# Optimization experiments

Hardware: AMD Instinct MI355X
Metric: run time of the kernel (lower is better)

Reference implementation:

```python
import jax, jax.numpy as jnp
import numpy as np

NEG_BIG = -1e9

def setup_inputs() -> dict:
    key = jax.random.key(0)
    kq, kk, kv, kwq, kwk, kwv, km = jax.random.split(key, 7)
    B, S, d = 16, 1024, 512
    Q = jax.random.normal(kq, (B, S, d), dtype=jnp.float32)
    K = jax.random.normal(kk, (B, S, d), dtype=jnp.float32)
    V = jax.random.normal(kv, (B, S, d), dtype=jnp.float32)
    # nn.Linear weights [d, d]; torch applies x @ W.T
    WQ = jax.random.normal(kwq, (d, d), dtype=jnp.float32) / np.sqrt(d)
    WK = jax.random.normal(kwk, (d, d), dtype=jnp.float32) / np.sqrt(d)
    WV = jax.random.normal(kwv, (d, d), dtype=jnp.float32) / np.sqrt(d)
    mask = jax.random.randint(km, (B, S), 0, 2, dtype=jnp.int32)
    return {"Q": Q, "K": K, "V": V, "WQ": WQ, "WK": WK, "WV": WV, "mask": mask}


def reference(Q, K, V, WQ, WK, WV, mask):
    d = Q.shape[-1]
    q = jnp.einsum('bsd,ed->bse', Q, WQ)
    k = jnp.einsum('bsd,ed->bse', K, WK)
    v = jnp.einsum('bsd,ed->bse', V, WV)
    scores = jnp.einsum('bqd,bkd->bqk', q, k) / jnp.sqrt(jnp.float32(d))
    attn = jax.nn.softmax(scores, axis=-1)
    # Faithful to original: mask applied AFTER softmax with -1e9 fill
    m = mask[:, None, :]  # [B,1,S] broadcast over query dim
    attn = jnp.where(m == 0, jnp.float32(NEG_BIG), attn)
    out = jnp.einsum('bqk,bkd->bqd', attn, v)
    return (out, attn)
```

## Files before the change

### kernel.cpp

```cpp
#include <hip/hip_runtime.h>
#include <hip/hip_bf16.h>

typedef float f32x4 __attribute__((ext_vector_type(4)));
typedef __bf16 bf16x8 __attribute__((ext_vector_type(8)));
typedef unsigned short u16x8 __attribute__((ext_vector_type(8)));
typedef unsigned short u16x4 __attribute__((ext_vector_type(4)));
typedef int i32x4 __attribute__((ext_vector_type(4)));

#define NEG_BIG_F (-1000000000.0f)
#define SCALE_F 0.044194173824159216f

__device__ __forceinline__ unsigned short f2bf(float f) {
  unsigned int u = __float_as_uint(f);
  u += 0x7FFFu + ((u >> 16) & 1u);
  return (unsigned short)(u >> 16);
}

__device__ __forceinline__ u16x8 cvt8(f32x4 a, f32x4 b) {
  u16x8 r;
  r[0] = f2bf(a[0]); r[1] = f2bf(a[1]); r[2] = f2bf(a[2]); r[3] = f2bf(a[3]);
  r[4] = f2bf(b[0]); r[5] = f2bf(b[1]); r[6] = f2bf(b[2]); r[7] = f2bf(b[3]);
  return r;
}

__device__ __forceinline__ bf16x8 u2b(u16x8 u) {
  union { u16x8 u; bf16x8 b; } c; c.u = u; return c.b;
}

__device__ __forceinline__ void gload16(const void* g, char* l) {
  __builtin_amdgcn_global_load_lds(
      (const __attribute__((address_space(1))) unsigned int*)g,
      (__attribute__((address_space(3))) unsigned int*)l, 16, 0, 0);
}

__global__ __launch_bounds__(256) void cvtW(
    const float* __restrict__ w0, const float* __restrict__ w1,
    const float* __restrict__ w2, unsigned short* __restrict__ out)
{
  const float* src = blockIdx.z == 0 ? w0 : (blockIdx.z == 1 ? w1 : w2);
  unsigned short* dst = out + (size_t)blockIdx.z * 262144;
  const int i = (blockIdx.x * 256 + threadIdx.x) * 8;
  f32x4 a = *(const f32x4*)(src + i);
  f32x4 b = *(const f32x4*)(src + i + 4);
  *(u16x8*)&dst[i] = cvt8(a, b);
}

__global__ __launch_bounds__(512, 2) void projqk(
    const float* __restrict__ Q, const float* __restrict__ Kx,
    const unsigned short* __restrict__ wb,
    unsigned short* __restrict__ qb, unsigned short* __restrict__ kb)
{
  __shared__ __align__(16) unsigned short As[2][256][32];
  __shared__ __align__(16) unsigned short Bs[2][256][32];

  const int tid = threadIdx.x, z = blockIdx.z;
  const float* X = z ? Kx : Q;
  const unsigned short* W = wb + (size_t)z * 262144;
  unsigned short* Y = z ? kb : qb;
  const int m0 = blockIdx.x * 256, n0 = blockIdx.y * 256;
  const int lane = tid & 63, wave = tid >> 6;
  const int wr = (wave >> 2) * 128, wc = (wave & 3) * 64;
  const int fr = lane & 15, fq = lane >> 4;

  f32x4 acc[8][4] = {};

  int arow_s[2], aswz_s[2];
  const float* gAs[2];
  #pragma unroll
  for (int i = 0; i < 2; i++) {
    const int c = tid + 512 * i;
    arow_s[i] = c >> 2;
    aswz_s[i] = ((c & 3) ^ ((arow_s[i] >> 1) & 3)) * 8;
    gAs[i] = X + (size_t)(m0 + arow_s[i]) * 512 + (c & 3) * 8;
  }
  const unsigned short* gB[2]; char* lB[2];
  #pragma unroll
  for (int i = 0; i < 2; i++) {
    const int c = tid + 512 * i, row = c >> 2, slot = c & 3;
    gB[i] = W + (size_t)(n0 + row) * 512 + (slot ^ ((row >> 1) & 3)) * 8;
    lB[i] = (char*)&Bs[0][0][0] + c * 16;
  }

  f32x4 pa[2][2];
  #pragma unroll
  for (int i = 0; i < 2; i++) {
    pa[i][0] = *(const f32x4*)(gAs[i]);
    pa[i][1] = *(const f32x4*)(gAs[i] + 4);
  }
  #pragma unroll
  for (int i = 0; i < 2; i++) gload16(gB[i], lB[i]);
  #pragma unroll
  for (int i = 0; i < 2; i++)
    *(u16x8*)&As[0][arow_s[i]][aswz_s[i]] = cvt8(pa[i][0], pa[i][1]);

  int cur = 0;
  for (int kt = 0; kt < 512; kt += 32) {
    const int nb = cur ^ 1;
    if (kt < 480) {
      #pragma unroll
      for (int i = 0; i < 2; i++) {
        pa[i][0] = *(const f32x4*)(gAs[i] + kt + 32);
        pa[i][1] = *(const f32x4*)(gAs[i] + kt + 36);
      }
      #pragma unroll
      for (int i = 0; i < 2; i++) gload16(gB[i] + kt + 32, lB[i] + nb * 16384);
      asm volatile("s_waitcnt vmcnt(6) lgkmcnt(0)" ::: "memory");
    } else {
      asm volatile("s_waitcnt vmcnt(0) lgkmcnt(0)" ::: "memory");
    }
    __builtin_amdgcn_sched_barrier(0);
    __builtin_amdgcn_s_barrier();

    bf16x8 bv[4];
    #pragma unroll
    for (int nf = 0; nf < 4; nf++) {
      const int br = wc + nf * 16 + fr;
      bv[nf] = *(const bf16x8*)&Bs[cur][br][(fq ^ ((br >> 1) & 3)) * 8];
    }
    #pragma unroll
    for (int mf = 0; mf < 8; mf++) {
      const int ar = wr + mf * 16 + fr;
      bf16x8 av = *(const bf16x8*)&As[cur][ar][(fq ^ ((ar >> 1) & 3)) * 8];
      #pragma unroll
      for (int nf = 0; nf < 4; nf++)
        acc[mf][nf] = __builtin_amdgcn_mfma_f32_16x16x32_bf16(av, bv[nf], acc[mf][nf], 0, 0, 0);
    }

    if (kt < 480) {
      #pragma unroll
      for (int i = 0; i < 2; i++)
        *(u16x8*)&As[nb][arow_s[i]][aswz_s[i]] = cvt8(pa[i][0], pa[i][1]);
    }
    __builtin_amdgcn_s_barrier();
    cur = nb;
  }

  #pragma unroll
  for (int mf = 0; mf < 8; mf++)
    #pragma unroll
    for (int nf = 0; nf < 4; nf++)
      #pragma unroll
      for (int rr = 0; rr < 4; rr++) {
        const int m = m0 + wr + mf * 16 + fq * 4 + rr;
        const int n = n0 + wc + nf * 16 + fr;
        Y[(size_t)m * 512 + n] = f2bf(acc[mf][nf][rr]);
      }
}

__global__ __launch_bounds__(512, 2) void projv(
    const float* __restrict__ V, const unsigned short* __restrict__ wv,
    unsigned short* __restrict__ vt)
{
  __shared__ __align__(16) unsigned short As[2][128][32];
  __shared__ __align__(16) unsigned short Bs[2][256][32];

  const int tid = threadIdx.x;
  const int m0 = blockIdx.x * 128, n0 = blockIdx.y * 256, b = blockIdx.z;
  const int lane = tid & 63, wave = tid >> 6;
  const int wr = (wave >> 2) * 64, wc = (wave & 3) * 64;
  const int fr = lane & 15, fq = lane >> 4;

  f32x4 acc[4][4] = {};

  const int ar_s = tid >> 2, aslot = tid & 3;
  const unsigned short* gA = wv + (size_t)(m0 + ar_s) * 512 + (aslot ^ ((ar_s >> 1) & 3)) * 8;
  char* lA = (char*)&As[0][0][0] + tid * 16;

  int brow_s[2], bswz_s[2];
  const float* gBs[2];
  #pragma unroll
  for (int i = 0; i < 2; i++) {
    const int c = tid + 512 * i;
    brow_s[i] = c >> 2;
    bswz_s[i] = ((c & 3) ^ ((brow_s[i] >> 1) & 3)) * 8;
    gBs[i] = V + ((size_t)b * 1024 + n0 + brow_s[i]) * 512 + (c & 3) * 8;
  }

  f32x4 pb[2][2];
  #pragma unroll
  for (int i = 0; i < 2; i++) {
    pb[i][0] = *(const f32x4*)(gBs[i]);
    pb[i][1] = *(const f32x4*)(gBs[i] + 4);
  }
  gload16(gA, lA);
  #pragma unroll
  for (int i = 0; i < 2; i++)
    *(u16x8*)&Bs[0][brow_s[i]][bswz_s[i]] = cvt8(pb[i][0], pb[i][1]);

  int cur = 0;
  for (int kt = 0; kt < 512; kt += 32) {
    const int nb = cur ^ 1;
    if (kt < 480) {
      #pragma unroll
      for (int i = 0; i < 2; i++) {
        pb[i][0] = *(const f32x4*)(gBs[i] + kt + 32);
        pb[i][1] = *(const f32x4*)(gBs[i] + kt + 36);
      }
      gload16(gA + kt + 32, lA + nb * 8192);
      asm volatile("s_waitcnt vmcnt(5) lgkmcnt(0)" ::: "memory");
    } else {
      asm volatile("s_waitcnt vmcnt(0) lgkmcnt(0)" ::: "memory");
    }
    __builtin_amdgcn_sched_barrier(0);
    __builtin_amdgcn_s_barrier();

    bf16x8 av[4], bv[4];
    #pragma unroll
    for (int mf = 0; mf < 4; mf++) {
      const int ar = wr + mf * 16 + fr;
      av[mf] = *(const bf16x8*)&As[cur][ar][(fq ^ ((ar >> 1) & 3)) * 8];
    }
    #pragma unroll
    for (int nf = 0; nf < 4; nf++) {
      const int br = wc + nf * 16 + fr;
      bv[nf] = *(const bf16x8*)&Bs[cur][br][(fq ^ ((br >> 1) & 3)) * 8];
    }
    #pragma unroll
    for (int mf = 0; mf < 4; mf++)
      #pragma unroll
      for (int nf = 0; nf < 4; nf++)
        acc[mf][nf] = __builtin_amdgcn_mfma_f32_16x16x32_bf16(av[mf], bv[nf], acc[mf][nf], 0, 0, 0);

    if (kt < 480) {
      #pragma unroll
      for (int i = 0; i < 2; i++)
        *(u16x8*)&Bs[nb][brow_s[i]][bswz_s[i]] = cvt8(pb[i][0], pb[i][1]);
    }
    __builtin_amdgcn_s_barrier();
    cur = nb;
  }

  #pragma unroll
  for (int mf = 0; mf < 4; mf++)
    #pragma unroll
    for (int nf = 0; nf < 4; nf++)
      #pragma unroll
      for (int rr = 0; rr < 4; rr++) {
        const int e = m0 + wr + mf * 16 + fq * 4 + rr;
        const int s = n0 + wc + nf * 16 + fr;
        vt[((size_t)b * 512 + e) * 1024 + s] = f2bf(acc[mf][nf][rr]);
      }
}

__global__ __launch_bounds__(512, 2) void score256(
    const unsigned short* __restrict__ qb, const unsigned short* __restrict__ kb,
    float* __restrict__ attn, float* __restrict__ partial)
{
  __shared__ __align__(16) unsigned short As[2][256][32];
  __shared__ __align__(16) unsigned short Bs[2][256][32];

  const int tid = threadIdx.x, bz = blockIdx.z;
  const int m0 = blockIdx.x * 256, n0 = blockIdx.y * 256;
  const int lane = tid & 63, wave = tid >> 6;
  const int wr = (wave >> 2) * 128, wc = (wave & 3) * 64;
  const int fr = lane & 15, fq = lane >> 4;

  f32x4 acc[8][4] = {};

  const unsigned short* gA[2]; char* lA[2];
  const unsigned short* gB[2]; char* lB[2];
  #pragma unroll
  for (int i = 0; i < 2; i++) {
    const int c = tid + 512 * i, row = c >> 2, slot = c & 3;
    const int sw = (slot ^ ((row >> 1) & 3)) * 8;
    gA[i] = qb + ((size_t)bz * 1024 + m0 + row) * 512 + sw;
    gB[i] = kb + ((size_t)bz * 1024 + n0 + row) * 512 + sw;
    lA[i] = (char*)&As[0][0][0] + c * 16;
    lB[i] = (char*)&Bs[0][0][0] + c * 16;
  }

  #pragma unroll
  for (int i = 0; i < 2; i++) { gload16(gA[i], lA[i]); gload16(gB[i], lB[i]); }

  int cur = 0;
  for (int kt = 0; kt < 512; kt += 32) {
    const int nb = cur ^ 1;
    if (kt < 480) {
      #pragma unroll
      for (int i = 0; i < 2; i++) {
        gload16(gA[i] + kt + 32, lA[i] + nb * 16384);
        gload16(gB[i] + kt + 32, lB[i] + nb * 16384);
      }
      asm volatile("s_waitcnt vmcnt(4) lgkmcnt(0)" ::: "memory");
    } else {
      asm volatile("s_waitcnt vmcnt(0) lgkmcnt(0)" ::: "memory");
    }
    __builtin_amdgcn_sched_barrier(0);
    __builtin_amdgcn_s_barrier();

    bf16x8 bv[4];
    #pragma unroll
    for (int nf = 0; nf < 4; nf++) {
      const int br = wc + nf * 16 + fr;
      bv[nf] = *(const bf16x8*)&Bs[cur][br][(fq ^ ((br >> 1) & 3)) * 8];
    }
    #pragma unroll
    for (int mf = 0; mf < 8; mf++) {
      const int ar = wr + mf * 16 + fr;
      bf16x8 av = *(const bf16x8*)&As[cur][ar][(fq ^ ((ar >> 1) & 3)) * 8];
      #pragma unroll
      for (int nf = 0; nf < 4; nf++)
        acc[mf][nf] = __builtin_amdgcn_mfma_f32_16x16x32_bf16(av, bv[nf], acc[mf][nf], 0, 0, 0);
    }
    __builtin_amdgcn_s_barrier();
    cur = nb;
  }

  float* Cb = attn + (size_t)bz * 1024 * 1024;
  const int slot = blockIdx.y * 4 + (wave & 3);
  #pragma unroll
  for (int mf = 0; mf < 8; mf++) {
    #pragma unroll
    for (int rr = 0; rr < 4; rr++) {
      const int m = m0 + wr + mf * 16 + fq * 4 + rr;
      float e = 0.f;
      #pragma unroll
      for (int nf = 0; nf < 4; nf++) {
        const float sv = acc[mf][nf][rr] * SCALE_F;
        Cb[(size_t)m * 1024 + n0 + wc + nf * 16 + fr] = sv;
        e += __expf(sv);
      }
      e += __shfl_xor(e, 1); e += __shfl_xor(e, 2);
      e += __shfl_xor(e, 4); e += __shfl_xor(e, 8);
      if (fr == 0)
        partial[(size_t)slot * 16384 + bz * 1024 + m] = e;
    }
  }
}

__global__ __launch_bounds__(256) void rs_inv(
    const float* __restrict__ partial, float* __restrict__ inv)
{
  const int i = blockIdx.x * 256 + threadIdx.x;
  float s = 0.f;
  #pragma unroll
  for (int p = 0; p < 16; p++) s += partial[(size_t)p * 16384 + i];
  inv[i] = 1.0f / s;
}

__global__ __launch_bounds__(512) void pv_gemm(
    float* __restrict__ attn, const unsigned short* __restrict__ vt,
    const float* __restrict__ inv, const int* __restrict__ mask,
    float* __restrict__ out)
{
  __shared__ __align__(16) unsigned short As[2][64][40];
  __shared__ __align__(16) unsigned short Bs[2][512][32];

  const int tid = threadIdx.x;
  const int bz = blockIdx.z, m0 = blockIdx.x * 64;
  const int lane = tid & 63, wave = tid >> 6;
  const int n0 = wave * 64;
  const int fr = lane & 15, fq = lane >> 4;

  f32x4 acc[4][4] = {};

  const int arow = tid >> 3, acol = (tid & 7) * 4;
  float* arp = attn + ((size_t)bz * 1024 + m0 + arow) * 1024 + acol;
  const float vinv = inv[bz * 1024 + m0 + arow];
  const int* mrow = mask + bz * 1024 + acol;

  const unsigned short* gB[4];
  char* lB[4];
  #pragma unroll
  for (int r = 0; r < 4; r++) {
    const int c = r * 512 + tid;
    const int row = c >> 2;
    gB[r] = vt + ((size_t)bz * 512 + row) * 1024 + ((c & 3) ^ ((row >> 1) & 3)) * 8;
    lB[r] = (char*)&Bs[0][0][0] + c * 16;
  }

  {
    f32x4 s = *(const f32x4*)(arp);
    i32x4 mv = *(const i32x4*)(mrow);
    f32x4 p;
    p[0] = mv[0] ? __expf(s[0]) * vinv : NEG_BIG_F;
    p[1] = mv[1] ? __expf(s[1]) * vinv : NEG_BIG_F;
    p[2] = mv[2] ? __expf(s[2]) * vinv : NEG_BIG_F;
    p[3] = mv[3] ? __expf(s[3]) * vinv : NEG_BIG_F;
    *(f32x4*)(arp) = p;
    u16x4 h;
    h[0] = f2bf(p[0]); h[1] = f2bf(p[1]); h[2] = f2bf(p[2]); h[3] = f2bf(p[3]);
    *(u16x4*)&As[0][arow][acol] = h;
    #pragma unroll
    for (int r = 0; r < 4; r++) gload16(gB[r], lB[r]);
  }
  __syncthreads();

  int cur = 0;
  for (int kt = 0; kt < 1024; kt += 32) {
    const int nb = cur ^ 1;
    f32x4 s; i32x4 mv;
    const bool more = (kt + 32) < 1024;
    if (more) {
      s = *(const f32x4*)(arp + kt + 32);
      mv = *(const i32x4*)(mrow + kt + 32);
      #pragma unroll
      for (int r = 0; r < 4; r++) gload16(gB[r] + kt + 32, lB[r] + nb * 32768);
    }

    bf16x8 af[4], bv[4];
    #pragma unroll
    for (int t = 0; t < 4; t++) {
      af[t] = *(const bf16x8*)&As[cur][t * 16 + fr][fq * 8];
      const int brow = n0 + t * 16 + fr;
      bv[t] = *(const bf16x8*)&Bs[cur][brow][(fq ^ ((brow >> 1) & 3)) * 8];
    }
    #pragma unroll
    for (int mt = 0; mt < 4; mt++)
      #pragma unroll
      for (int nt = 0; nt < 4; nt++)
        acc[mt][nt] = __builtin_amdgcn_mfma_f32_16x16x32_bf16(af[mt], bv[nt], acc[mt][nt], 0, 0, 0);

    if (more) {
      f32x4 p;
      p[0] = mv[0] ? __expf(s[0]) * vinv : NEG_BIG_F;
      p[1] = mv[1] ? __expf(s[1]) * vinv : NEG_BIG_F;
      p[2] = mv[2] ? __expf(s[2]) * vinv : NEG_BIG_F;
      p[3] = mv[3] ? __expf(s[3]) * vinv : NEG_BIG_F;
      *(f32x4*)(arp + kt + 32) = p;
      u16x4 h;
      h[0] = f2bf(p[0]); h[1] = f2bf(p[1]); h[2] = f2bf(p[2]); h[3] = f2bf(p[3]);
      *(u16x4*)&As[nb][arow][acol] = h;
    }
    __syncthreads();
    cur = nb;
  }

  #pragma unroll
  for (int mt = 0; mt < 4; mt++)
    #pragma unroll
    for (int nt = 0; nt < 4; nt++)
      #pragma unroll
      for (int rr = 0; rr < 4; rr++)
        out[((size_t)bz * 1024 + m0 + mt * 16 + fq * 4 + rr) * 512 + n0 + nt * 16 + fr] =
            acc[mt][nt][rr];
}

extern "C" void kernel_launch(void* const* d_in, const int* in_sizes, int n_in,
                              void* d_out, int out_size, void* d_ws, size_t ws_size,
                              hipStream_t stream)
{
  const float* Q  = (const float*)d_in[0];
  const float* Kx = (const float*)d_in[1];
  const float* V  = (const float*)d_in[2];
  const float* WQ = (const float*)d_in[3];
  const float* WK = (const float*)d_in[4];
  const float* WV = (const float*)d_in[5];
  const int* mask = (const int*)d_in[6];

  const int B = 16, S = 1024, D = 512;
  float* out_f  = (float*)d_out;
  float* attn_f = out_f + (size_t)B * S * D;

  unsigned short* qb = (unsigned short*)d_ws;
  unsigned short* kb = qb + (size_t)B * S * D;
  unsigned short* vt = kb + (size_t)B * S * D;
  unsigned short* wb = vt + (size_t)B * S * D;
  float* partial = (float*)(wb + 786432);
  float* inv = partial + 262144;

  cvtW<<<dim3(128, 1, 3), 256, 0, stream>>>(WQ, WK, WV, wb);
  projqk<<<dim3(64, 2, 2), 512, 0, stream>>>(Q, Kx, wb, qb, kb);
  projv<<<dim3(4, 4, 16), 512, 0, stream>>>(V, wb + 524288, vt);
  score256<<<dim3(4, 4, 16), 512, 0, stream>>>(qb, kb, attn_f, partial);
  rs_inv<<<dim3(64), 256, 0, stream>>>(partial, inv);
  pv_gemm<<<dim3(16, 1, 16), 512, 0, stream>>>(attn_f, vt, inv, mask, out_f);
}
```

Measured before the change: 163.5 us.

## Store masked unnormalized bf16 probabilities and fold the mask term algebraically into the PV output

score256 now applies exp and the mask and writes unnormalized bf16 probabilities into the output buffer, instead of writing fp32 scores. A separate attn_write kernel builds the normalized fp32 attn output from them. pv_gemm streams that bf16 P with async global_load_lds double buffering and adds the contribution of the -1e9 masked entries algebraically, using a per-column masked V sum from a new mvsum_k kernel. The aim is to cut the fp32 read-modify-write of the full attention matrix and the per-element exp inside the GEMM loop. In exchange it adds two kernel launches, reuses the output memory as scratch (safe only because each block reads exactly the rows it later overwrites), and changes rounding of the large masked term.

```diff
diff --git a/kernel.cpp b/kernel.cpp
--- a/kernel.cpp
+++ b/kernel.cpp
@@ -4,7 +4,6 @@
 typedef float f32x4 __attribute__((ext_vector_type(4)));
 typedef __bf16 bf16x8 __attribute__((ext_vector_type(8)));
 typedef unsigned short u16x8 __attribute__((ext_vector_type(8)));
-typedef unsigned short u16x4 __attribute__((ext_vector_type(4)));
 typedef int i32x4 __attribute__((ext_vector_type(4)));
 
 #define NEG_BIG_F (-1000000000.0f)
@@ -14,6 +13,10 @@
   unsigned int u = __float_as_uint(f);
   u += 0x7FFFu + ((u >> 16) & 1u);
   return (unsigned short)(u >> 16);
+}
+
+__device__ __forceinline__ float bf2f(unsigned short h) {
+  return __uint_as_float((unsigned int)h << 16);
 }
 
 __device__ __forceinline__ u16x8 cvt8(f32x4 a, f32x4 b) {
@@ -21,10 +24,6 @@
   r[0] = f2bf(a[0]); r[1] = f2bf(a[1]); r[2] = f2bf(a[2]); r[3] = f2bf(a[3]);
   r[4] = f2bf(b[0]); r[5] = f2bf(b[1]); r[6] = f2bf(b[2]); r[7] = f2bf(b[3]);
   return r;
-}
-
-__device__ __forceinline__ bf16x8 u2b(u16x8 u) {
-  union { u16x8 u; bf16x8 b; } c; c.u = u; return c.b;
 }
 
 __device__ __forceinline__ void gload16(const void* g, char* l) {
@@ -244,7 +243,8 @@
 
 __global__ __launch_bounds__(512, 2) void score256(
     const unsigned short* __restrict__ qb, const unsigned short* __restrict__ kb,
-    float* __restrict__ attn, float* __restrict__ partial)
+    const int* __restrict__ mask,
+    unsigned short* __restrict__ P, float* __restrict__ partial)
 {
   __shared__ __align__(16) unsigned short As[2][256][32];
   __shared__ __align__(16) unsigned short Bs[2][256][32];
@@ -306,7 +306,12 @@
     cur = nb;
   }
 
-  float* Cb = attn + (size_t)bz * 1024 * 1024;
+  int mcol[4];
+  #pragma unroll
+  for (int nf = 0; nf < 4; nf++)
+    mcol[nf] = mask[bz * 1024 + n0 + wc + nf * 16 + fr];
+
+  unsigned short* Pb = P + ((size_t)bz << 20);
   const int slot = blockIdx.y * 4 + (wave & 3);
   #pragma unroll
   for (int mf = 0; mf < 8; mf++) {
@@ -316,9 +321,10 @@
       float e = 0.f;
       #pragma unroll
       for (int nf = 0; nf < 4; nf++) {
-        const float sv = acc[mf][nf][rr] * SCALE_F;
-        Cb[(size_t)m * 1024 + n0 + wc + nf * 16 + fr] = sv;
-        e += __expf(sv);
+        const float ev = __expf(acc[mf][nf][rr] * SCALE_F);
+        e += ev;
+        Pb[(size_t)m * 1024 + n0 + wc + nf * 16 + fr] =
+            mcol[nf] ? f2bf(ev) : (unsigned short)0;
       }
       e += __shfl_xor(e, 1); e += __shfl_xor(e, 2);
       e += __shfl_xor(e, 4); e += __shfl_xor(e, 8);
@@ -338,12 +344,60 @@
   inv[i] = 1.0f / s;
 }
 
+__global__ __launch_bounds__(256) void mvsum_k(
+    const unsigned short* __restrict__ vt, const int* __restrict__ mask,
+    float* __restrict__ mvsum)
+{
+  const int row = blockIdx.x * 4 + (threadIdx.x >> 6);
+  const int b = row >> 9;
+  const int lane = threadIdx.x & 63;
+  const unsigned short* vr = vt + (size_t)row * 1024 + lane * 16;
+  const int* mr = mask + b * 1024 + lane * 16;
+  u16x8 v0 = *(const u16x8*)(vr);
+  u16x8 v1 = *(const u16x8*)(vr + 8);
+  float s = 0.f;
+  #pragma unroll
+  for (int j = 0; j < 8; j++) {
+    if (!mr[j])     s += bf2f(v0[j]);
+    if (!mr[8 + j]) s += bf2f(v1[j]);
+  }
+  #pragma unroll
+  for (int o = 32; o > 0; o >>= 1) s += __shfl_xor(s, o);
+  if (lane == 0) mvsum[row] = s;
+}
+
+__global__ __launch_bounds__(256) void attn_write(
+    const unsigned short* __restrict__ P, const float* __restrict__ inv,
+    const int* __restrict__ mask, float* __restrict__ attn)
+{
+  const size_t base = ((size_t)blockIdx.x * 256 + threadIdx.x) * 8;
+  const int row = (int)(base >> 10);
+  const int b = row >> 10;
+  const int k0 = (int)(base & 1023);
+  const u16x8 p8 = *(const u16x8*)(P + base);
+  const float iv = inv[row];
+  const int* mr = mask + b * 1024 + k0;
+  const i32x4 ma = *(const i32x4*)(mr);
+  const i32x4 mb = *(const i32x4*)(mr + 4);
+  f32x4 o0, o1;
+  o0[0] = ma[0] ? bf2f(p8[0]) * iv : NEG_BIG_F;
+  o0[1] = ma[1] ? bf2f(p8[1]) * iv : NEG_BIG_F;
+  o0[2] = ma[2] ? bf2f(p8[2]) * iv : NEG_BIG_F;
+  o0[3] = ma[3] ? bf2f(p8[3]) * iv : NEG_BIG_F;
+  o1[0] = mb[0] ? bf2f(p8[4]) * iv : NEG_BIG_F;
+  o1[1] = mb[1] ? bf2f(p8[5]) * iv : NEG_BIG_F;
+  o1[2] = mb[2] ? bf2f(p8[6]) * iv : NEG_BIG_F;
+  o1[3] = mb[3] ? bf2f(p8[7]) * iv : NEG_BIG_F;
+  *(f32x4*)(attn + base) = o0;
+  *(f32x4*)(attn + base + 4) = o1;
+}
+
 __global__ __launch_bounds__(512) void pv_gemm(
-    float* __restrict__ attn, const unsigned short* __restrict__ vt,
-    const float* __restrict__ inv, const int* __restrict__ mask,
+    const unsigned short* __restrict__ P, const unsigned short* __restrict__ vt,
+    const float* __restrict__ inv, const float* __restrict__ mvsum,
     float* __restrict__ out)
 {
-  __shared__ __align__(16) unsigned short As[2][64][40];
+  __shared__ __align__(16) unsigned short As[2][64][32];
   __shared__ __align__(16) unsigned short Bs[2][512][32];
 
   const int tid = threadIdx.x;
@@ -354,86 +408,75 @@
 
   f32x4 acc[4][4] = {};
 
-  const int arow = tid >> 3, acol = (tid & 7) * 4;
-  float* arp = attn + ((size_t)bz * 1024 + m0 + arow) * 1024 + acol;
-  const float vinv = inv[bz * 1024 + m0 + arow];
-  const int* mrow = mask + bz * 1024 + acol;
-
-  const unsigned short* gB[4];
-  char* lB[4];
-  #pragma unroll
-  for (int r = 0; r < 4; r++) {
-    const int c = r * 512 + tid;
-    const int row = c >> 2;
-    gB[r] = vt + ((size_t)bz * 512 + row) * 1024 + ((c & 3) ^ ((row >> 1) & 3)) * 8;
-    lB[r] = (char*)&Bs[0][0][0] + c * 16;
-  }
-
-  {
-    f32x4 s = *(const f32x4*)(arp);
-    i32x4 mv = *(const i32x4*)(mrow);
-    f32x4 p;
-    p[0] = mv[0] ? __expf(s[0]) * vinv : NEG_BIG_F;
-    p[1] = mv[1] ? __expf(s[1]) * vinv : NEG_BIG_F;
-    p[2] = mv[2] ? __expf(s[2]) * vinv : NEG_BIG_F;
-    p[3] = mv[3] ? __expf(s[3]) * vinv : NEG_BIG_F;
-    *(f32x4*)(arp) = p;
-    u16x4 h;
-    h[0] = f2bf(p[0]); h[1] = f2bf(p[1]); h[2] = f2bf(p[2]); h[3] = f2bf(p[3]);
-    *(u16x4*)&As[0][arow][acol] = h;
-    #pragma unroll
-    for (int r = 0; r < 4; r++) gload16(gB[r], lB[r]);
-  }
-  __syncthreads();
+  const unsigned short* gA = nullptr; char* lA = nullptr;
+  if (tid < 256) {
+    const int row = tid >> 2, slot = tid & 3;
+    gA = P + ((size_t)bz << 20) + (size_t)(m0 + row) * 1024 + (slot ^ ((row >> 1) & 3)) * 8;
+    lA = (char*)&As[0][0][0] + tid * 16;
+  }
+  const unsigned short* gB[4]; char* lB[4];
+  #pragma unroll
+  for (int i = 0; i < 4; i++) {
+    const int c = tid + 512 * i, row = c >> 2, slot = c & 3;
+    gB[i] = vt + ((size_t)bz * 512 + row) * 1024 + (slot ^ ((row >> 1) & 3)) * 8;
+    lB[i] = (char*)&Bs[0][0][0] + c * 16;
+  }
+
+  if (tid < 256) gload16(gA, lA);
+  #pragma unroll
+  for (int i = 0; i < 4; i++) gload16(gB[i], lB[i]);
 
   int cur = 0;
-  for (int kt = 0; kt < 1024; kt += 32) {
+  for (int t = 0; t < 32; t++) {
     const int nb = cur ^ 1;
-    f32x4 s; i32x4 mv;
-    const bool more = (kt + 32) < 1024;
-    if (more) {
-      s = *(const f32x4*)(arp + kt + 32);
-      mv = *(const i32x4*)(mrow + kt + 32);
-      #pragma unroll
-      for (int r = 0; r < 4; r++) gload16(gB[r] + kt + 32, lB[r] + nb * 32768);
-    }
+    const int kt = t * 32;
+    if (t < 31) {
+      if (tid < 256) gload16(gA + kt + 32, lA + nb * 4096);
+      #pragma unroll
+      for (int i = 0; i < 4; i++) gload16(gB[i] + kt + 32, lB[i] + nb * 32768);
+      if (wave < 4) asm volatile("s_waitcnt vmcnt(5) lgkmcnt(0)" ::: "memory");
+      else          asm volatile("s_waitcnt vmcnt(4) lgkmcnt(0)" ::: "memory");
+    } else {
+      asm volatile("s_waitcnt vmcnt(0) lgkmcnt(0)" ::: "memory");
+    }
+    __builtin_amdgcn_sched_barrier(0);
+    __builtin_amdgcn_s_barrier();
 
     bf16x8 af[4], bv[4];
     #pragma unroll
-    for (int t = 0; t < 4; t++) {
-      af[t] = *(const bf16x8*)&As[cur][t * 16 + fr][fq * 8];
-      const int brow = n0 + t * 16 + fr;
-      bv[t] = *(const bf16x8*)&Bs[cur][brow][(fq ^ ((brow >> 1) & 3)) * 8];
-    }
-    #pragma unroll
-    for (int mt = 0; mt < 4; mt++)
-      #pragma unroll
-      for (int nt = 0; nt < 4; nt++)
-        acc[mt][nt] = __builtin_amdgcn_mfma_f32_16x16x32_bf16(af[mt], bv[nt], acc[mt][nt], 0, 0, 0);
-
-    if (more) {
-      f32x4 p;
-      p[0] = mv[0] ? __expf(s[0]) * vinv : NEG_BIG_F;
-      p[1] = mv[1] ? __expf(s[1]) * vinv : NEG_BIG_F;
-      p[2] = mv[2] ? __expf(s[2]) * vinv : NEG_BIG_F;
-      p[3] = mv[3] ? __expf(s[3]) * vinv : NEG_BIG_F;
-      *(f32x4*)(arp + kt + 32) = p;
-      u16x4 h;
-      h[0] = f2bf(p[0]); h[1] = f2bf(p[1]); h[2] = f2bf(p[2]); h[3] = f2bf(p[3]);
-      *(u16x4*)&As[nb][arow][acol] = h;
-    }
-    __syncthreads();
+    for (int mf = 0; mf < 4; mf++) {
+      const int ar = mf * 16 + fr;
+      af[mf] = *(const bf16x8*)&As[cur][ar][(fq ^ ((ar >> 1) & 3)) * 8];
+    }
+    #pragma unroll
+    for (int nf = 0; nf < 4; nf++) {
+      const int br = n0 + nf * 16 + fr;
+      bv[nf] = *(const bf16x8*)&Bs[cur][br][(fq ^ ((br >> 1) & 3)) * 8];
+    }
+    #pragma unroll
+    for (int mf = 0; mf < 4; mf++)
+      #pragma unroll
+      for (int nf = 0; nf < 4; nf++)
+        acc[mf][nf] = __builtin_amdgcn_mfma_f32_16x16x32_bf16(af[mf], bv[nf], acc[mf][nf], 0, 0, 0);
+    __builtin_amdgcn_s_barrier();
     cur = nb;
   }
 
-  #pragma unroll
-  for (int mt = 0; mt < 4; mt++)
-    #pragma unroll
-    for (int nt = 0; nt < 4; nt++)
-      #pragma unroll
-      for (int rr = 0; rr < 4; rr++)
-        out[((size_t)bz * 1024 + m0 + mt * 16 + fq * 4 + rr) * 512 + n0 + nt * 16 + fr] =
-            acc[mt][nt][rr];
+  float mvv[4];
+  #pragma unroll
+  for (int nf = 0; nf < 4; nf++)
+    mvv[nf] = mvsum[bz * 512 + n0 + nf * 16 + fr];
+  #pragma unroll
+  for (int mf = 0; mf < 4; mf++)
+    #pragma unroll
+    for (int rr = 0; rr < 4; rr++) {
+      const int m = m0 + mf * 16 + fq * 4 + rr;
+      const float iv = inv[bz * 1024 + m];
+      #pragma unroll
+      for (int nf = 0; nf < 4; nf++)
+        out[((size_t)bz * 1024 + m) * 512 + n0 + nf * 16 + fr] =
+            iv * acc[mf][nf][rr] + NEG_BIG_F * mvv[nf];
+    }
 }
 
 extern "C" void kernel_launch(void* const* d_in, const int* in_sizes, int n_in,
@@ -451,6 +494,7 @@
   const int B = 16, S = 1024, D = 512;
   float* out_f  = (float*)d_out;
   float* attn_f = out_f + (size_t)B * S * D;
+  unsigned short* Pbuf = (unsigned short*)d_out;
 
   unsigned short* qb = (unsigned short*)d_ws;
   unsigned short* kb = qb + (size_t)B * S * D;
@@ -458,11 +502,14 @@
   unsigned short* wb = vt + (size_t)B * S * D;
   float* partial = (float*)(wb + 786432);
   float* inv = partial + 262144;
+  float* mvsum = inv + 16384;
 
   cvtW<<<dim3(128, 1, 3), 256, 0, stream>>>(WQ, WK, WV, wb);
   projqk<<<dim3(64, 2, 2), 512, 0, stream>>>(Q, Kx, wb, qb, kb);
   projv<<<dim3(4, 4, 16), 512, 0, stream>>>(V, wb + 524288, vt);
-  score256<<<dim3(4, 4, 16), 512, 0, stream>>>(qb, kb, attn_f, partial);
+  score256<<<dim3(4, 4, 16), 512, 0, stream>>>(qb, kb, mask, Pbuf, partial);
   rs_inv<<<dim3(64), 256, 0, stream>>>(partial, inv);
-  pv_gemm<<<dim3(16, 1, 16), 512, 0, stream>>>(attn_f, vt, inv, mask, out_f);
-}
+  mvsum_k<<<dim3(2048), 256, 0, stream>>>(vt, mask, mvsum);
+  attn_write<<<dim3(8192), 256, 0, stream>>>(Pbuf, inv, mask, attn_f);
+  pv_gemm<<<dim3(16, 1, 16), 512, 0, stream>>>(Pbuf, vt, inv, mvsum, out_f);
+}
```

Result: no change. 166.2 us (+1.6%).
